# Optimization experiments

Measured on AMD Instinct MI355X. Metric: run time of the kernel, lower is better.

## Reference

```python
import jax, jax.numpy as jnp
import numpy as np

N = 50000
E = 800000
IN_DIM = 256
OUT_DIM = 64
ALPHA = 0.2  # LeakyReLU negative slope
EPS = 9e-15


def setup_inputs() -> dict:
    key = jax.random.key(0)
    k1, k2, k3, k4 = jax.random.split(key, 4)
    x = jax.random.normal(k1, (N, IN_DIM), dtype=jnp.float32)
    edge = jax.random.randint(k2, (2, E), 0, N, dtype=jnp.int32)
    # xavier_normal with gain=1.414
    gain = 1.414
    W = jax.random.normal(k3, (IN_DIM, OUT_DIM), dtype=jnp.float32) * (gain * np.sqrt(2.0 / (IN_DIM + OUT_DIM)))
    attn = jax.random.normal(k4, (1, 2 * OUT_DIM), dtype=jnp.float32) * (gain * np.sqrt(2.0 / (1 + 2 * OUT_DIM)))
    return {"x": x, "edge": edge, "W": W, "attn": attn}


def reference(x, edge, W, attn):
    n = x.shape[0]
    h = x @ W                                   # [N, D]
    src, dst = edge[0], edge[1]
    d = h.shape[1]
    a_src = attn[0, :d]                         # attn . concat(h_src, h_dst) split
    a_dst = attn[0, d:]
    s = h @ a_src                               # [N]
    t = h @ a_dst                               # [N]
    values = s[src] + t[dst]                    # [E] per-edge attention logits
    edge_e_a = jnp.where(values >= 0, values, ALPHA * values)  # LeakyReLU
    edge_e = jnp.exp(edge_e_a - jnp.max(edge_e_a))              # [E]
    # scatter-sum over destination rows (edge[0] is the output row in spmm)
    e_rowsum = jax.ops.segment_sum(edge_e, src, num_segments=n)[:, None]  # [N,1]
    msgs = edge_e[:, None] * h[dst]             # [E, D] gathered messages
    h_prime = jax.ops.segment_sum(msgs, src, num_segments=n)              # [N, D]
    h_prime = h_prime / (e_rowsum + EPS)
    return h_prime
```

## Files before the change

kernel.cpp:

```cpp
#include <hip/hip_runtime.h>
#include <stdint.h>

#define NN 50000
#define NE 800000
#define KDIM 256
#define DDIM 64
#define ALPHA 0.2f
#define EPSV 9e-15f

#define NBIN 512
#define BSPAN 98
#define SPAN2 49
#define BCAP 2048
#define HCAP 1024
#define PBLK 256
#define EPB 3125
#define GEMM_BLOCKS 1024
#define FGRID (PBLK + GEMM_BLOCKS)

#define O_S    0
#define O_T    50000
#define O_HB   100000
#define O_WB   1700000
#define O_BIN  1708192
#define O_EBUF 1708704

typedef __bf16 bf16x8 __attribute__((ext_vector_type(8)));
typedef float f32x4 __attribute__((ext_vector_type(4)));

__device__ __forceinline__ ushort f2bf(float f) {
    uint32_t u = __float_as_uint(f);
    return (ushort)((u + 0x7fffu + ((u >> 16) & 1u)) >> 16);
}
__device__ __forceinline__ float bf2f(ushort u) {
    return __uint_as_float(((uint32_t)u) << 16);
}
__device__ __forceinline__ uint binof(uint src) {
    return (src * 85599u) >> 23;
}

__global__ __launch_bounds__(256) void k_prep(const float* __restrict__ W,
                                              uint* __restrict__ BINCNT,
                                              uint4* __restrict__ WB) {
    const int g = blockIdx.x * 256 + threadIdx.x;
    if (g < NBIN) BINCNT[g] = 0u;
    if (g < 2048) {
        int ts = g >> 6;
        int ln = g & 63;
        int s = ts >> 2, t = ts & 3;
        int q = ln >> 4, c = ln & 15;
        union { ushort us[8]; uint4 v; } pk;
#pragma unroll
        for (int j = 0; j < 8; ++j) {
            int k = s * 32 + q * 8 + j;
            pk.us[j] = f2bf(W[k * DDIM + t * 16 + c]);
        }
        WB[g] = pk.v;
    }
}

__global__ __launch_bounds__(256) void k_fused(const float* __restrict__ X,
                                               const uint4* __restrict__ WB,
                                               const float* __restrict__ attn,
                                               const int* __restrict__ edge,
                                               ushort* __restrict__ HB,
                                               float* __restrict__ S,
                                               float* __restrict__ T,
                                               uint* __restrict__ BINCNT,
                                               uint* __restrict__ EBUF) {
    __shared__ uint4 bsm[2048];

    if (blockIdx.x < PBLK) {
        uint* sm = (uint*)bsm;
        const int CNT0 = 0, BST = 512, GBS = 1024, STG = 1536, SRT = 4672;
        const int tid = threadIdx.x;
        const int p0 = blockIdx.x * EPB;
        for (int b = tid; b < NBIN; b += 256) sm[CNT0 + b] = 0u;
        __syncthreads();
        for (int k = tid; k < EPB; k += 256) {
            uint s = (uint)edge[p0 + k];
            uint d = (uint)edge[NE + p0 + k];
            sm[STG + k] = s | (d << 16);
            atomicAdd(&sm[CNT0 + binof(s)], 1u);
        }
        __syncthreads();
        if (tid < 64) {
            uint carry = 0;
            for (int c = 0; c < 8; ++c) {
                uint v = sm[CNT0 + c * 64 + tid];
                uint incl = v;
#pragma unroll
                for (int m = 1; m < 64; m <<= 1) {
                    uint t = __shfl_up(incl, m, 64);
                    if (tid >= m) incl += t;
                }
                sm[BST + c * 64 + tid] = incl - v + carry;
                carry += __shfl(incl, 63, 64);
            }
        }
        __syncthreads();
        for (int b = tid; b < NBIN; b += 256) {
            uint c = sm[CNT0 + b];
            sm[GBS + b] = c ? atomicAdd(&BINCNT[b], c) : 0u;
            sm[CNT0 + b] = sm[BST + b];
        }
        __syncthreads();
        for (int k = tid; k < EPB; k += 256) {
            uint pk = sm[STG + k];
            uint bin = binof(pk & 0xffffu);
            uint slot = atomicAdd(&sm[CNT0 + bin], 1u);
            sm[SRT + slot] = pk;
        }
        __syncthreads();
        for (int k = tid; k < EPB; k += 256) {
            uint pk = sm[SRT + k];
            uint bin = binof(pk & 0xffffu);
            uint local = (uint)k - sm[BST + bin] + sm[GBS + bin];
            if (local < BCAP) EBUF[bin * BCAP + local] = pk;
        }
        return;
    }

    uint4 wreg[8];
#pragma unroll
    for (int j = 0; j < 8; ++j) wreg[j] = WB[j * 256 + threadIdx.x];
#pragma unroll
    for (int j = 0; j < 8; ++j) bsm[j * 256 + threadIdx.x] = wreg[j];
    __syncthreads();

    const int lane = threadIdx.x & 63;
    const int wave = (blockIdx.x - PBLK) * 4 + (threadIdx.x >> 6);
    const int nwaves = GEMM_BLOCKS * 4;
    const int quad = lane >> 4;
    const int nn = lane & 15;

    float asrc[4], adst[4];
#pragma unroll
    for (int t = 0; t < 4; ++t) {
        asrc[t] = attn[t * 16 + nn];
        adst[t] = attn[DDIM + t * 16 + nn];
    }

    const int MT = NN / 16;
    for (int mt = wave; mt < MT; mt += nwaves) {
        const int row0 = mt * 16;
        const float* xr = X + (size_t)(row0 + nn) * KDIM + quad * 8;
        bf16x8 afrag[8];
#pragma unroll
        for (int s = 0; s < 8; ++s) {
            float4 lo = *reinterpret_cast<const float4*>(xr + s * 32);
            float4 hi = *reinterpret_cast<const float4*>(xr + s * 32 + 4);
            union { uint u[4]; bf16x8 v; } aa;
            asm("v_cvt_pk_bf16_f32 %0, %1, %2"
                : "=v"(aa.u[0]) : "v"(lo.x), "v"(lo.y));
            asm("v_cvt_pk_bf16_f32 %0, %1, %2"
                : "=v"(aa.u[1]) : "v"(lo.z), "v"(lo.w));
            asm("v_cvt_pk_bf16_f32 %0, %1, %2"
                : "=v"(aa.u[2]) : "v"(hi.x), "v"(hi.y));
            asm("v_cvt_pk_bf16_f32 %0, %1, %2"
                : "=v"(aa.u[3]) : "v"(hi.z), "v"(hi.w));
            afrag[s] = aa.v;
        }

        f32x4 acc[4];
#pragma unroll
        for (int t = 0; t < 4; ++t) acc[t] = {0.f, 0.f, 0.f, 0.f};
#pragma unroll
        for (int s = 0; s < 8; ++s)
#pragma unroll
            for (int t = 0; t < 4; ++t) {
                bf16x8 bf = *reinterpret_cast<const bf16x8*>(
                    &bsm[(s * 4 + t) * 64 + lane]);
                acc[t] = __builtin_amdgcn_mfma_f32_16x16x32_bf16(
                    afrag[s], bf, acc[t], 0, 0, 0);
            }

#pragma unroll
        for (int t = 0; t < 4; ++t)
#pragma unroll
            for (int r = 0; r < 4; ++r)
                HB[(size_t)(row0 + quad * 4 + r) * DDIM + t * 16 + nn] =
                    f2bf(acc[t][r]);

        float sp[4], tp[4];
#pragma unroll
        for (int r = 0; r < 4; ++r) { sp[r] = 0.f; tp[r] = 0.f; }
#pragma unroll
        for (int t = 0; t < 4; ++t)
#pragma unroll
            for (int r = 0; r < 4; ++r) {
                sp[r] = fmaf(acc[t][r], asrc[t], sp[r]);
                tp[r] = fmaf(acc[t][r], adst[t], tp[r]);
            }
#pragma unroll
        for (int m = 1; m < 16; m <<= 1)
#pragma unroll
            for (int r = 0; r < 4; ++r) {
                sp[r] += __shfl_xor(sp[r], m, 64);
                tp[r] += __shfl_xor(tp[r], m, 64);
            }
        if (nn == 0) {
#pragma unroll
            for (int r = 0; r < 4; ++r) {
                S[row0 + quad * 4 + r] = sp[r];
                T[row0 + quad * 4 + r] = tp[r];
            }
        }
    }
}

__global__ __launch_bounds__(512) void k_agg(const uint* __restrict__ EBUF,
                                             const uint* __restrict__ BINCNT,
                                             const float* __restrict__ S,
                                             const float* __restrict__ T,
                                             const ushort* __restrict__ HB,
                                             float* __restrict__ out) {
    __shared__ uint2 sDE[HCAP];
    __shared__ uint  cntL[SPAN2];
    __shared__ uint  off[SPAN2 + 1];
    __shared__ uint  cur[SPAN2];
    __shared__ float Sseg[SPAN2];

    const int b = blockIdx.x >> 1;
    const int half = blockIdx.x & 1;
    const int nb0 = b * BSPAN + half * SPAN2;
    const int tid = threadIdx.x;

    if (tid < SPAN2) {
        cntL[tid] = 0u;
        int node = nb0 + tid;
        Sseg[tid] = (node < NN) ? S[node] : 0.f;
    }
    __syncthreads();

    int cnt = (int)BINCNT[b];
    cnt = cnt < BCAP ? cnt : BCAP;
    const uint* eb = EBUF + b * BCAP;

    for (int k = tid; k < cnt; k += 512) {
        int row = (int)(eb[k] & 0xffffu) - nb0;
        if ((unsigned)row < SPAN2) atomicAdd(&cntL[row], 1u);
    }
    __syncthreads();

    if (tid < 64) {
        uint v = (tid < SPAN2) ? cntL[tid] : 0u;
        uint incl = v;
#pragma unroll
        for (int m = 1; m < 64; m <<= 1) {
            uint t = __shfl_up(incl, m, 64);
            if (tid >= m) incl += t;
        }
        if (tid < SPAN2) { off[tid] = incl - v; cur[tid] = incl - v; }
        if (tid == SPAN2 - 1) off[SPAN2] = incl;
    }
    __syncthreads();

    for (int k = tid; k < cnt; k += 512) {
        uint pk = eb[k];
        int row = (int)(pk & 0xffffu) - nb0;
        if ((unsigned)row < SPAN2) {
            float v = Sseg[row] + T[pk >> 16];
            float a = v >= 0.f ? v : ALPHA * v;
            float e = __expf(a);
            uint pos = atomicAdd(&cur[row], 1u);
            sDE[pos] = make_uint2(pk >> 16, __float_as_uint(e));
        }
    }
    __syncthreads();

    const int wv = tid >> 6;
    const int lane = tid & 63;
    const int sub = lane >> 5;
    const int c2 = lane & 31;
    const ushort* hb2 = HB + 2 * c2;

    for (int r = wv; r < SPAN2; r += 8) {
        const int start = (int)off[r];
        const int deg = (int)(off[r + 1] - off[r]);
        float a0 = 0.f, a1 = 0.f, rs = 0.f;
        for (int j = 0; j < deg; j += 16) {
            uint dd[8]; float ee[8];
#pragma unroll
            for (int u = 0; u < 8; ++u) {
                int idx = j + 2 * u + sub;
                int ic = start + (idx < deg ? idx : 0);
                uint2 q = sDE[ic];
                dd[u] = q.x;
                ee[u] = (idx < deg) ? __uint_as_float(q.y) : 0.f;
            }
            __builtin_amdgcn_sched_barrier(0);
            float f0[8], f1[8];
#pragma unroll
            for (int u = 0; u < 8; ++u) {
                uint g2 = *reinterpret_cast<const uint*>(
                    hb2 + (size_t)dd[u] * DDIM);
                f0[u] = bf2f((ushort)(g2 & 0xffffu));
                f1[u] = bf2f((ushort)(g2 >> 16));
            }
            __builtin_amdgcn_sched_barrier(0);
#pragma unroll
            for (int u = 0; u < 8; ++u) {
                a0 = fmaf(ee[u], f0[u], a0);
                a1 = fmaf(ee[u], f1[u], a1);
                rs += ee[u];
            }
        }
        a0 += __shfl_xor(a0, 32, 64);
        a1 += __shfl_xor(a1, 32, 64);
        rs += __shfl_xor(rs, 32, 64);
        const int node = nb0 + r;
        if (sub == 0 && node < NN) {
            float inv = 1.f / (rs + EPSV);
            reinterpret_cast<float2*>(out + (size_t)node * DDIM)[c2] =
                make_float2(a0 * inv, a1 * inv);
        }
    }
}

extern "C" void kernel_launch(void* const* d_in, const int* in_sizes, int n_in,
                              void* d_out, int out_size, void* d_ws, size_t ws_size,
                              hipStream_t stream) {
    const float* X    = (const float*)d_in[0];
    const int*   edge = (const int*)d_in[1];
    const float* W    = (const float*)d_in[2];
    const float* attn = (const float*)d_in[3];

    uint*   wu = (uint*)d_ws;
    float*  wf = (float*)d_ws;
    float*  S      = wf + O_S;
    float*  T      = wf + O_T;
    ushort* HB     = (ushort*)(wu + O_HB);
    uint4*  WB     = (uint4*)(wu + O_WB);
    uint*   BINCNT = wu + O_BIN;
    uint*   EBUF   = wu + O_EBUF;

    k_prep<<<8, 256, 0, stream>>>(W, BINCNT, WB);
    k_fused<<<FGRID, 256, 0, stream>>>(X, WB, attn, edge, HB, S, T, BINCNT, EBUF);
    k_agg<<<NBIN * 2, 512, 0, stream>>>(EBUF, BINCNT, S, T, HB, (float*)d_out);
}
```

Measured before the change: 126.4 us.

## Use 512-thread fused blocks and 4-edge-per-wave aggregation with 8-byte gathers

The fused partition/GEMM kernel now runs with 512 threads per block and half as many GEMM blocks, so the partition blocks process edges with twice the threads and each GEMM block loads the shared W copy once for eight waves. Separately, the aggregation inner loop is restructured so each wave processes four edges at a time with 16 lanes per edge, each lane gathering 4 bf16 features (uint2) instead of 2. This is meant to widen the per-lane memory transactions and cut the number of gather instructions. The trade-off is more shuffle reduction steps, more partial accumulators per lane, and fewer total waves per dimension-lane for low-degree rows.

```diff
diff --git a/kernel.cpp b/kernel.cpp
--- a/kernel.cpp
+++ b/kernel.cpp
@@ -15,7 +15,7 @@
 #define HCAP 1024
 #define PBLK 256
 #define EPB 3125
-#define GEMM_BLOCKS 1024
+#define GEMM_BLOCKS 512
 #define FGRID (PBLK + GEMM_BLOCKS)
 
 #define O_S    0
@@ -59,7 +59,7 @@
     }
 }
 
-__global__ __launch_bounds__(256) void k_fused(const float* __restrict__ X,
+__global__ __launch_bounds__(512) void k_fused(const float* __restrict__ X,
                                                const uint4* __restrict__ WB,
                                                const float* __restrict__ attn,
                                                const int* __restrict__ edge,
@@ -75,9 +75,9 @@
         const int CNT0 = 0, BST = 512, GBS = 1024, STG = 1536, SRT = 4672;
         const int tid = threadIdx.x;
         const int p0 = blockIdx.x * EPB;
-        for (int b = tid; b < NBIN; b += 256) sm[CNT0 + b] = 0u;
-        __syncthreads();
-        for (int k = tid; k < EPB; k += 256) {
+        for (int b = tid; b < NBIN; b += 512) sm[CNT0 + b] = 0u;
+        __syncthreads();
+        for (int k = tid; k < EPB; k += 512) {
             uint s = (uint)edge[p0 + k];
             uint d = (uint)edge[NE + p0 + k];
             sm[STG + k] = s | (d << 16);
@@ -99,20 +99,20 @@
             }
         }
         __syncthreads();
-        for (int b = tid; b < NBIN; b += 256) {
+        for (int b = tid; b < NBIN; b += 512) {
             uint c = sm[CNT0 + b];
             sm[GBS + b] = c ? atomicAdd(&BINCNT[b], c) : 0u;
             sm[CNT0 + b] = sm[BST + b];
         }
         __syncthreads();
-        for (int k = tid; k < EPB; k += 256) {
+        for (int k = tid; k < EPB; k += 512) {
             uint pk = sm[STG + k];
             uint bin = binof(pk & 0xffffu);
             uint slot = atomicAdd(&sm[CNT0 + bin], 1u);
             sm[SRT + slot] = pk;
         }
         __syncthreads();
-        for (int k = tid; k < EPB; k += 256) {
+        for (int k = tid; k < EPB; k += 512) {
             uint pk = sm[SRT + k];
             uint bin = binof(pk & 0xffffu);
             uint local = (uint)k - sm[BST + bin] + sm[GBS + bin];
@@ -121,16 +121,16 @@
         return;
     }
 
-    uint4 wreg[8];
-#pragma unroll
-    for (int j = 0; j < 8; ++j) wreg[j] = WB[j * 256 + threadIdx.x];
-#pragma unroll
-    for (int j = 0; j < 8; ++j) bsm[j * 256 + threadIdx.x] = wreg[j];
+    uint4 wreg[4];
+#pragma unroll
+    for (int j = 0; j < 4; ++j) wreg[j] = WB[j * 512 + threadIdx.x];
+#pragma unroll
+    for (int j = 0; j < 4; ++j) bsm[j * 512 + threadIdx.x] = wreg[j];
     __syncthreads();
 
     const int lane = threadIdx.x & 63;
-    const int wave = (blockIdx.x - PBLK) * 4 + (threadIdx.x >> 6);
-    const int nwaves = GEMM_BLOCKS * 4;
+    const int wave = (blockIdx.x - PBLK) * 8 + (threadIdx.x >> 6);
+    const int nwaves = GEMM_BLOCKS * 8;
     const int quad = lane >> 4;
     const int nn = lane & 15;
 
@@ -271,49 +271,53 @@
 
     const int wv = tid >> 6;
     const int lane = tid & 63;
-    const int sub = lane >> 5;
-    const int c2 = lane & 31;
-    const ushort* hb2 = HB + 2 * c2;
+    const int sub4 = lane >> 4;
+    const int c4 = lane & 15;
+    const ushort* hb4 = HB + 4 * c4;
 
     for (int r = wv; r < SPAN2; r += 8) {
         const int start = (int)off[r];
         const int deg = (int)(off[r + 1] - off[r]);
-        float a0 = 0.f, a1 = 0.f, rs = 0.f;
+        float a0 = 0.f, a1 = 0.f, a2 = 0.f, a3 = 0.f, rs = 0.f;
         for (int j = 0; j < deg; j += 16) {
-            uint dd[8]; float ee[8];
-#pragma unroll
-            for (int u = 0; u < 8; ++u) {
-                int idx = j + 2 * u + sub;
+            uint dd[4]; float ee[4];
+#pragma unroll
+            for (int u = 0; u < 4; ++u) {
+                int idx = j + 4 * u + sub4;
                 int ic = start + (idx < deg ? idx : 0);
                 uint2 q = sDE[ic];
                 dd[u] = q.x;
                 ee[u] = (idx < deg) ? __uint_as_float(q.y) : 0.f;
             }
             __builtin_amdgcn_sched_barrier(0);
-            float f0[8], f1[8];
-#pragma unroll
-            for (int u = 0; u < 8; ++u) {
-                uint g2 = *reinterpret_cast<const uint*>(
-                    hb2 + (size_t)dd[u] * DDIM);
-                f0[u] = bf2f((ushort)(g2 & 0xffffu));
-                f1[u] = bf2f((ushort)(g2 >> 16));
-            }
+            uint2 g[4];
+#pragma unroll
+            for (int u = 0; u < 4; ++u)
+                g[u] = *reinterpret_cast<const uint2*>(
+                    hb4 + (size_t)dd[u] * DDIM);
             __builtin_amdgcn_sched_barrier(0);
 #pragma unroll
-            for (int u = 0; u < 8; ++u) {
-                a0 = fmaf(ee[u], f0[u], a0);
-                a1 = fmaf(ee[u], f1[u], a1);
+            for (int u = 0; u < 4; ++u) {
+                a0 = fmaf(ee[u], bf2f((ushort)(g[u].x & 0xffffu)), a0);
+                a1 = fmaf(ee[u], bf2f((ushort)(g[u].x >> 16)), a1);
+                a2 = fmaf(ee[u], bf2f((ushort)(g[u].y & 0xffffu)), a2);
+                a3 = fmaf(ee[u], bf2f((ushort)(g[u].y >> 16)), a3);
                 rs += ee[u];
             }
         }
-        a0 += __shfl_xor(a0, 32, 64);
-        a1 += __shfl_xor(a1, 32, 64);
-        rs += __shfl_xor(rs, 32, 64);
+#pragma unroll
+        for (int m = 16; m < 64; m <<= 1) {
+            a0 += __shfl_xor(a0, m, 64);
+            a1 += __shfl_xor(a1, m, 64);
+            a2 += __shfl_xor(a2, m, 64);
+            a3 += __shfl_xor(a3, m, 64);
+            rs += __shfl_xor(rs, m, 64);
+        }
         const int node = nb0 + r;
-        if (sub == 0 && node < NN) {
+        if (sub4 == 0 && node < NN) {
             float inv = 1.f / (rs + EPSV);
-            reinterpret_cast<float2*>(out + (size_t)node * DDIM)[c2] =
-                make_float2(a0 * inv, a1 * inv);
+            float4 o = make_float4(a0 * inv, a1 * inv, a2 * inv, a3 * inv);
+            *reinterpret_cast<float4*>(out + (size_t)node * DDIM + 4 * c4) = o;
         }
     }
 }
@@ -336,6 +340,6 @@
     uint*   EBUF   = wu + O_EBUF;
 
     k_prep<<<8, 256, 0, stream>>>(W, BINCNT, WB);
-    k_fused<<<FGRID, 256, 0, stream>>>(X, WB, attn, edge, HB, S, T, BINCNT, EBUF);
+    k_fused<<<FGRID, 512, 0, stream>>>(X, WB, attn, edge, HB, S, T, BINCNT, EBUF);
     k_agg<<<NBIN * 2, 512, 0, stream>>>(EBUF, BINCNT, S, T, HB, (float*)d_out);
 }
```

Result: faster. 122.8 us, median of 3 (-2.8%).
